# Optimization experiments

Hardware: AMD Instinct MI355X
Metric: run time of the kernel (lower is better)

The kernel has to match this reference:

```python
import jax, jax.numpy as jnp
import numpy as np

TS = 1.5          # hard-coded sampling period in forward()
W_CENTER = 337.927  # hard-coded center frequency in forward()


def shg_mat(yta):
    """Vectorized createSHGmat: yta is a complex64 vector of length N.
    Row m: Ts * fftshift(fft(fftshift(yta * roll(yta, delay[m]) * shiftFactor))).
    torch.roll(x, s)[j] == x[(j - s) % N], matching the gather below."""
    N = yta.shape[0]
    delays_f = jnp.arange(-(N // 2), N // 2, dtype=jnp.float32)
    delays_i = jnp.arange(-(N // 2), N // 2, dtype=jnp.int32)
    shift_factor = jnp.exp(-1j * 2.0 * W_CENTER * TS * delays_f).astype(jnp.complex64)  # [N]
    idx = (jnp.arange(N, dtype=jnp.int32)[None, :] - delays_i[:, None]) % N  # [N, N]
    y_shift = yta[idx]                                    # [N(delay), N(elem)]
    prod = yta[None, :] * y_shift * shift_factor[None, :]  # elementwise, [N, N]
    prod = jnp.fft.fftshift(prod, axes=-1)
    mat = TS * jnp.fft.fftshift(jnp.fft.fft(prod, axis=-1), axes=-1)
    return mat  # complex64 [N, N]


def frog_error(Tref, Tmeas):
    """calcFrogError: scalar FROG error between reference and measured traces."""
    mu = jnp.sum(Tmeas @ Tref) / jnp.sum(Tref @ Tref)
    r = jnp.sum((Tmeas - mu * Tref) ** 2)
    norm = jnp.float32(Tmeas.size) * jnp.max(Tmeas) ** 2
    return jnp.sqrt(r / norm)


def setup_inputs() -> dict:
    key = jax.random.key(0)
    k1, k2, k3 = jax.random.split(key, 3)
    B, N = 8, 1024
    prediction = jax.random.normal(k1, (B, 2 * N), dtype=jnp.float32)
    label = jax.random.normal(k2, (B, 2 * N), dtype=jnp.float32)
    spectrogram = jax.random.uniform(k3, (N, N), dtype=jnp.float32)
    return {"prediction": prediction, "label": label, "spectrogram": spectrogram}


def reference(prediction, label, spectrogram):
    B, two_n = prediction.shape
    n = two_n // 2
    pred_analytical = (prediction[:, :n] + 1j * prediction[:, n:]).astype(jnp.complex64)  # [B, N]
    mats = jax.vmap(shg_mat)(pred_analytical)          # [B, N, N] complex64
    Tref = jnp.abs(mats)                               # predicted SHG trace magnitude
    errs = jax.vmap(lambda t: frog_error(t, spectrogram))(Tref)  # [B]
    # loss = (sum over batch of frog_error) / batch_size; masked MSE terms in the
    # original are computed but never added to the returned loss, so they are omitted.
    return jnp.mean(errs)
```

## Files before the change

kernel.cpp:

```cpp
#include <hip/hip_runtime.h>
#include <math.h>

#define N 1024
#define B_ 8
#define T_ 256
#define R_ 8
#define NREP 4

#define OFF_SF      0
#define OFF_TW      2048
#define OFF_ROWSUM  10240
#define ZERO_START  18432
#define OFF_COLSUMM 18432
#define OFF_SUMM2   19456
#define OFF_MAXM    19457
#define OFF_SUMMT   19464
#define OFF_SUMTT   19472
#define OFF_COLT    20480
#define WS_END      (OFF_COLT + B_ * NREP * N)

#define S1(a) ((a) ^ (((a) >> 2) & 0x10))
#define S2(a) ((a) ^ (((a) >> 3) & 0x0C))
#define S3(a) ((a) ^ (((a) >> 5) & 0x07))
#define S4(a) ((a) ^ (((a) >> 5) & 0x07))

__device__ __forceinline__ float wave_sum(float v) {
    #pragma unroll
    for (int o = 32; o > 0; o >>= 1) v += __shfl_down(v, o, 64);
    return v;
}
__device__ __forceinline__ float wave_max(float v) {
    #pragma unroll
    for (int o = 32; o > 0; o >>= 1) v = fmaxf(v, __shfl_down(v, o, 64));
    return v;
}

__device__ __forceinline__ void load_tw(float tw[6], const float* __restrict__ p) {
    float4 v = *(const float4*)p;
    float2 w = *(const float2*)(p + 4);
    tw[0] = v.x; tw[1] = v.y; tw[2] = v.z; tw[3] = v.w; tw[4] = w.x; tw[5] = w.y;
}

__device__ __forceinline__ void bfly4(float xr[4], float xi[4], const float tw[6]) {
    float t0r = xr[0] + xr[2], t0i = xi[0] + xi[2];
    float t1r = xr[0] - xr[2], t1i = xi[0] - xi[2];
    float t2r = xr[1] + xr[3], t2i = xi[1] + xi[3];
    float t3r = xr[1] - xr[3], t3i = xi[1] - xi[3];
    float y1r = t1r + t3i, y1i = t1i - t3r;
    float y2r = t0r - t2r, y2i = t0i - t2i;
    float y3r = t1r - t3i, y3i = t1i + t3r;
    xr[0] = t0r + t2r;            xi[0] = t0i + t2i;
    xr[1] = y1r * tw[0] - y1i * tw[1]; xi[1] = y1r * tw[1] + y1i * tw[0];
    xr[2] = y2r * tw[2] - y2i * tw[3]; xi[2] = y2r * tw[3] + y2i * tw[2];
    xr[3] = y3r * tw[4] - y3i * tw[5]; xi[3] = y3r * tw[5] + y3i * tw[4];
}

__global__ __launch_bounds__(T_) void k_prep(float* ws) {
    const int e = blockIdx.x * T_ + threadIdx.x;
    {
        double ang = -2.0 * 337.927 * 1.5 * (double)(e - 512);
        double s, c;
        sincos(ang, &s, &c);
        ws[OFF_SF + 2 * e] = (float)c;
        ws[OFF_SF + 2 * e + 1] = (float)s;
    }
    {
        int s = e >> 8, tt = e & 255;
        int h = 256 >> (2 * s);
        int pos = tt & (h - 1);
        int step = 1 << (2 * s);
        double a1 = -2.0 * M_PI * (double)(pos * step) / 1024.0;
        double s1, c1, s2, c2, s3, c3;
        sincos(a1, &s1, &c1);
        sincos(2.0 * a1, &s2, &c2);
        sincos(3.0 * a1, &s3, &c3);
        float* p = ws + OFF_TW + e * 8;
        p[0] = (float)c1; p[1] = (float)s1;
        p[2] = (float)c2; p[3] = (float)s2;
        p[4] = (float)c3; p[5] = (float)s3;
        p[6] = 0.f; p[7] = 0.f;
    }
}

__global__ __launch_bounds__(T_) void k_mstats(const float* __restrict__ M, float* ws) {
    const int t = threadIdx.x;
    const int r0 = blockIdx.x * 16;
    float cs[4] = {0.f, 0.f, 0.f, 0.f};
    float sq = 0.f, mx = 0.f;
    for (int r = 0; r < 16; ++r) {
        const float* row = M + (size_t)(r0 + r) * N;
        #pragma unroll
        for (int q = 0; q < 4; ++q) {
            float v = row[t + T_ * q];
            cs[q] += v;
            sq += v * v;
            mx = fmaxf(mx, v);
        }
    }
    #pragma unroll
    for (int q = 0; q < 4; ++q) atomicAdd(&ws[OFF_COLSUMM + t + T_ * q], cs[q]);
    sq = wave_sum(sq);
    mx = wave_max(mx);
    __shared__ float rs_[4], rm_[4];
    int wid = t >> 6, lane = t & 63;
    if (lane == 0) { rs_[wid] = sq; rm_[wid] = mx; }
    __syncthreads();
    if (t == 0) {
        atomicAdd(&ws[OFF_SUMM2], rs_[0] + rs_[1] + rs_[2] + rs_[3]);
        float X = fmaxf(fmaxf(rm_[0], rm_[1]), fmaxf(rm_[2], rm_[3]));
        atomicMax((unsigned int*)ws + OFF_MAXM, __float_as_uint(X));
    }
}

__global__ __launch_bounds__(T_, 4) void k_row(const float* __restrict__ pred,
                                               const float* __restrict__ M,
                                               float* __restrict__ ws) {
    __shared__ float Yr[N], Yi[N];
    __shared__ float Ar[N], Ai[N], Br[N], Bi[N];
    __shared__ float colA[N];
    __shared__ float red[3][4];
    const int t = threadIdx.x;
    const int m0 = blockIdx.x * R_;
    const int b = blockIdx.y;
    const int wid = t >> 6, lane = t & 63;

    {
        const float* pr = pred + (size_t)b * 2 * N;
        #pragma unroll
        for (int q = 0; q < 4; ++q) {
            int j = t + T_ * q;
            Yr[j] = pr[j];
            Yi[j] = pr[N + j];
            colA[j] = 0.f;
        }
    }
    __syncthreads();

    float mtacc = 0.f, ttacc = 0.f;
    float xr[4], xi[4], tw[6];

    for (int r = 0; r < R_; ++r) {
        const int m = m0 + r;

        {
            const float2* sf2 = (const float2*)(ws + OFF_SF);
            #pragma unroll
            for (int q = 0; q < 4; ++q) {
                int j = t + T_ * q;
                int s = (j - m + 512) & (N - 1);
                float ar = Yr[j], ai = Yi[j];
                float br = Yr[s], bi = Yi[s];
                float2 sv = sf2[j];
                float p_r = ar * br - ai * bi;
                float p_i = ar * bi + ai * br;
                xr[q] = p_r * sv.x - p_i * sv.y;
                xi[q] = p_r * sv.y + p_i * sv.x;
            }
            load_tw(tw, ws + OFF_TW + (size_t)t * 8);
            bfly4(xr, xi, tw);
            #pragma unroll
            for (int q = 0; q < 4; ++q) { int a = t + 256 * q; Ar[a] = xr[q]; Ai[a] = xi[q]; }
        }
        __syncthreads();

        {
            int base = ((t >> 6) << 8) | (t & 63);
            #pragma unroll
            for (int q = 0; q < 4; ++q) { int a = base + (q << 6); xr[q] = Ar[a]; xi[q] = Ai[a]; }
            load_tw(tw, ws + OFF_TW + (size_t)(256 + t) * 8);
            bfly4(xr, xi, tw);
            #pragma unroll
            for (int q = 0; q < 4; ++q) { int a = S1(base + (q << 6)); Br[a] = xr[q]; Bi[a] = xi[q]; }
        }
        __syncthreads();

        {
            int base = ((t >> 4) << 6) | (t & 15);
            #pragma unroll
            for (int q = 0; q < 4; ++q) { int a = S1(base + (q << 4)); xr[q] = Br[a]; xi[q] = Bi[a]; }
            load_tw(tw, ws + OFF_TW + (size_t)(512 + t) * 8);
            bfly4(xr, xi, tw);
            #pragma unroll
            for (int q = 0; q < 4; ++q) { int a = S2(base + (q << 4)); Ar[a] = xr[q]; Ai[a] = xi[q]; }
        }
        __syncthreads();

        {
            int base = ((t >> 2) << 4) | (t & 3);
            #pragma unroll
            for (int q = 0; q < 4; ++q) { int a = S2(base + (q << 2)); xr[q] = Ar[a]; xi[q] = Ai[a]; }
            load_tw(tw, ws + OFF_TW + (size_t)(768 + t) * 8);
            bfly4(xr, xi, tw);
            #pragma unroll
            for (int q = 0; q < 4; ++q) { int a = S3(base + (q << 2)); Br[a] = xr[q]; Bi[a] = xi[q]; }
        }
        __syncthreads();

        {
            int base = t << 2;
            #pragma unroll
            for (int q = 0; q < 4; ++q) { int a = S3(base + q); xr[q] = Br[a]; xi[q] = Bi[a]; }
            float t0r = xr[0] + xr[2], t0i = xi[0] + xi[2];
            float t1r = xr[0] - xr[2], t1i = xi[0] - xi[2];
            float t2r = xr[1] + xr[3], t2i = xi[1] + xi[3];
            float t3r = xr[1] - xr[3], t3i = xi[1] - xi[3];
            float yr[4], yi[4];
            yr[0] = t0r + t2r; yi[0] = t0i + t2i;
            yr[1] = t1r + t3i; yi[1] = t1i - t3r;
            yr[2] = t0r - t2r; yi[2] = t0i - t2i;
            yr[3] = t1r - t3i; yi[3] = t1i + t3r;
            int r4t = ((t & 3) << 6) | (((t >> 2) & 3) << 4) | (((t >> 4) & 3) << 2) | ((t >> 6) & 3);
            #pragma unroll
            for (int q = 0; q < 4; ++q) {
                int c = ((q << 8) | r4t) ^ 512;
                Ar[S4(c)] = 1.5f * sqrtf(yr[q] * yr[q] + yi[q] * yi[q]);
            }
        }
        __syncthreads();

        {
            const float* Mrow = M + (size_t)m * N;
            float rs = 0.f;
            #pragma unroll
            for (int q = 0; q < 4; ++q) {
                int cc = t + 256 * q;
                float v = Ar[S4(cc)];
                rs += v;
                ttacc += v * v;
                mtacc += Mrow[cc] * v;
                colA[cc] += v;
            }
            rs = wave_sum(rs);
            if (lane == 0) red[0][wid] = rs;
            __syncthreads();
            if (t == 0) {
                ws[OFF_ROWSUM + b * N + m] = red[0][0] + red[0][1] + red[0][2] + red[0][3];
            }
        }
    }

    {
        float* colT = ws + OFF_COLT + (size_t)(b * NREP + (blockIdx.x & (NREP - 1))) * N;
        #pragma unroll
        for (int q = 0; q < 4; ++q) {
            int cc = t + 256 * q;
            atomicAdd(&colT[cc], colA[cc]);
        }
        float mt = wave_sum(mtacc);
        float tt2 = wave_sum(ttacc);
        if (lane == 0) { red[1][wid] = mt; red[2][wid] = tt2; }
        __syncthreads();
        if (t == 0) {
            atomicAdd(&ws[OFF_SUMMT + b], red[1][0] + red[1][1] + red[1][2] + red[1][3]);
            atomicAdd(&ws[OFF_SUMTT + b], red[2][0] + red[2][1] + red[2][2] + red[2][3]);
        }
    }
}

__global__ __launch_bounds__(T_) void k_final(float* ws, float* out) {
    __shared__ double redn[4], redd[4];
    const int b = blockIdx.x;
    const int t = threadIdx.x;
    const int wid = t >> 6, lane = t & 63;
    const float* rowsum = ws + OFF_ROWSUM + (size_t)b * N;
    double num = 0.0, den = 0.0;
    #pragma unroll
    for (int q = 0; q < 4; ++q) {
        int j = t + 256 * q;
        double r = (double)rowsum[j];
        float ct = 0.f;
        #pragma unroll
        for (int rep = 0; rep < NREP; ++rep)
            ct += ws[OFF_COLT + (size_t)(b * NREP + rep) * N + j];
        num += (double)ws[OFF_COLSUMM + j] * r;
        den += (double)ct * r;
    }
    #pragma unroll
    for (int o = 32; o > 0; o >>= 1) {
        num += __shfl_down(num, o, 64);
        den += __shfl_down(den, o, 64);
    }
    if (lane == 0) { redn[wid] = num; redd[wid] = den; }
    __syncthreads();
    if (t == 0) {
        double NUM = redn[0] + redn[1] + redn[2] + redn[3];
        double DEN = redd[0] + redd[1] + redd[2] + redd[3];
        double mu = NUM / DEN;
        double r = (double)ws[OFF_SUMM2] - 2.0 * mu * (double)ws[OFF_SUMMT + b]
                 + mu * mu * (double)ws[OFF_SUMTT + b];
        float mx = ws[OFF_MAXM];
        double norm = 1048576.0 * (double)mx * (double)mx;
        atomicAdd(out, (float)(sqrt(r / norm) / 8.0));
    }
}

extern "C" void kernel_launch(void* const* d_in, const int* in_sizes, int n_in,
                              void* d_out, int out_size, void* d_ws, size_t ws_size,
                              hipStream_t stream) {
    const float* pred = (const float*)d_in[0];
    const float* M = (const float*)d_in[2];
    float* ws = (float*)d_ws;
    float* out = (float*)d_out;

    hipMemsetAsync(ws + ZERO_START, 0, (size_t)(WS_END - ZERO_START) * sizeof(float), stream);
    hipMemsetAsync(out, 0, sizeof(float), stream);
    k_prep<<<4, T_, 0, stream>>>(ws);
    k_mstats<<<64, T_, 0, stream>>>(M, ws);
    dim3 grid(N / R_, B_);
    k_row<<<grid, T_, 0, stream>>>(pred, M, ws);
    k_final<<<B_, T_, 0, stream>>>(ws, out);
}
```

Before: 106.0 us.

## Exploit row symmetry m↔N−m, fuse M stats into row kernel, drop memsets

Uses the magnitude symmetry between delay rows m and N−m so each block computes only rows 0..512 and reuses the FFT magnitudes for the mirrored row, weighting the trace sums accordingly. The spectrogram statistics (column sums, sum of squares, max) move from a separate kernel into the batch-0 blocks of the row kernel, and the workspace and output zeroing moves from memset calls into the prep kernel. Together these cut the FFT work roughly in half and remove three launches. In exchange the b==0 blocks read two M rows and carry extra branches, and the grid now has 129 columns with an uneven final block.

Result: no change. 105.3 us (-0.6%).

```diff
diff --git a/kernel.cpp b/kernel.cpp
--- a/kernel.cpp
+++ b/kernel.cpp
@@ -4,8 +4,9 @@
 #define N 1024
 #define B_ 8
 #define T_ 256
-#define R_ 8
+#define R_ 4
 #define NREP 4
+#define GX 129
 
 #define OFF_SF      0
 #define OFF_TW      2048
@@ -55,7 +56,7 @@
     xr[3] = y3r * tw[4] - y3i * tw[5]; xi[3] = y3r * tw[5] + y3i * tw[4];
 }
 
-__global__ __launch_bounds__(T_) void k_prep(float* ws) {
+__global__ __launch_bounds__(T_) void k_prep(float* ws, float* out) {
     const int e = blockIdx.x * T_ + threadIdx.x;
     {
         double ang = -2.0 * 337.927 * 1.5 * (double)(e - 512);
@@ -80,36 +81,8 @@
         p[4] = (float)c3; p[5] = (float)s3;
         p[6] = 0.f; p[7] = 0.f;
     }
-}
-
-__global__ __launch_bounds__(T_) void k_mstats(const float* __restrict__ M, float* ws) {
-    const int t = threadIdx.x;
-    const int r0 = blockIdx.x * 16;
-    float cs[4] = {0.f, 0.f, 0.f, 0.f};
-    float sq = 0.f, mx = 0.f;
-    for (int r = 0; r < 16; ++r) {
-        const float* row = M + (size_t)(r0 + r) * N;
-        #pragma unroll
-        for (int q = 0; q < 4; ++q) {
-            float v = row[t + T_ * q];
-            cs[q] += v;
-            sq += v * v;
-            mx = fmaxf(mx, v);
-        }
-    }
-    #pragma unroll
-    for (int q = 0; q < 4; ++q) atomicAdd(&ws[OFF_COLSUMM + t + T_ * q], cs[q]);
-    sq = wave_sum(sq);
-    mx = wave_max(mx);
-    __shared__ float rs_[4], rm_[4];
-    int wid = t >> 6, lane = t & 63;
-    if (lane == 0) { rs_[wid] = sq; rm_[wid] = mx; }
-    __syncthreads();
-    if (t == 0) {
-        atomicAdd(&ws[OFF_SUMM2], rs_[0] + rs_[1] + rs_[2] + rs_[3]);
-        float X = fmaxf(fmaxf(rm_[0], rm_[1]), fmaxf(rm_[2], rm_[3]));
-        atomicMax((unsigned int*)ws + OFF_MAXM, __float_as_uint(X));
-    }
+    for (int j = ZERO_START + e; j < WS_END; j += 4 * T_) ws[j] = 0.f;
+    if (e == 0) out[0] = 0.f;
 }
 
 __global__ __launch_bounds__(T_, 4) void k_row(const float* __restrict__ pred,
@@ -117,11 +90,13 @@
                                                float* __restrict__ ws) {
     __shared__ float Yr[N], Yi[N];
     __shared__ float Ar[N], Ai[N], Br[N], Bi[N];
-    __shared__ float colA[N];
-    __shared__ float red[3][4];
+    __shared__ float colA[N], colM[N];
+    __shared__ float red[5][4];
     const int t = threadIdx.x;
-    const int m0 = blockIdx.x * R_;
+    const int blk = blockIdx.x;
     const int b = blockIdx.y;
+    const int nr = (blk == GX - 1) ? 1 : R_;
+    const int m0 = blk * R_;
     const int wid = t >> 6, lane = t & 63;
 
     {
@@ -132,15 +107,18 @@
             Yr[j] = pr[j];
             Yi[j] = pr[N + j];
             colA[j] = 0.f;
+            colM[j] = 0.f;
         }
     }
     __syncthreads();
 
-    float mtacc = 0.f, ttacc = 0.f;
+    float mtacc = 0.f, ttacc = 0.f, sqacc = 0.f, mxacc = 0.f;
     float xr[4], xi[4], tw[6];
 
-    for (int r = 0; r < R_; ++r) {
+    for (int r = 0; r < nr; ++r) {
         const int m = m0 + r;
+        const int mm = (N - m) & (N - 1);
+        const float w = (mm == m) ? 1.f : 2.f;
 
         {
             const float2* sf2 = (const float2*)(ws + OFF_SF);
@@ -220,39 +198,72 @@
 
         {
             const float* Mrow = M + (size_t)m * N;
+            const float* Mrow2 = M + (size_t)mm * N;
             float rs = 0.f;
             #pragma unroll
             for (int q = 0; q < 4; ++q) {
                 int cc = t + 256 * q;
                 float v = Ar[S4(cc)];
                 rs += v;
-                ttacc += v * v;
-                mtacc += Mrow[cc] * v;
-                colA[cc] += v;
+                ttacc += w * v * v;
+                float m1 = Mrow[cc];
+                float msum = m1;
+                if (mm != m) msum += Mrow2[cc];
+                mtacc += msum * v;
+                colA[cc] += w * v;
+                if (b == 0) {
+                    colM[cc] += msum;
+                    sqacc += m1 * m1;
+                    mxacc = fmaxf(mxacc, m1);
+                    if (mm != m) {
+                        float m2 = msum - m1;
+                        sqacc += m2 * m2;
+                        mxacc = fmaxf(mxacc, m2);
+                    }
+                }
             }
             rs = wave_sum(rs);
             if (lane == 0) red[0][wid] = rs;
             __syncthreads();
             if (t == 0) {
-                ws[OFF_ROWSUM + b * N + m] = red[0][0] + red[0][1] + red[0][2] + red[0][3];
+                float R = red[0][0] + red[0][1] + red[0][2] + red[0][3];
+                ws[OFF_ROWSUM + b * N + m] = R;
+                if (mm != m) ws[OFF_ROWSUM + b * N + mm] = R;
             }
         }
     }
 
     {
-        float* colT = ws + OFF_COLT + (size_t)(b * NREP + (blockIdx.x & (NREP - 1))) * N;
+        float* colT = ws + OFF_COLT + (size_t)(b * NREP + (blk & (NREP - 1))) * N;
         #pragma unroll
         for (int q = 0; q < 4; ++q) {
             int cc = t + 256 * q;
             atomicAdd(&colT[cc], colA[cc]);
         }
+        if (b == 0) {
+            #pragma unroll
+            for (int q = 0; q < 4; ++q) {
+                int cc = t + 256 * q;
+                atomicAdd(&ws[OFF_COLSUMM + cc], colM[cc]);
+            }
+        }
         float mt = wave_sum(mtacc);
         float tt2 = wave_sum(ttacc);
         if (lane == 0) { red[1][wid] = mt; red[2][wid] = tt2; }
+        if (b == 0) {
+            float sq = wave_sum(sqacc);
+            float mx = wave_max(mxacc);
+            if (lane == 0) { red[3][wid] = sq; red[4][wid] = mx; }
+        }
         __syncthreads();
         if (t == 0) {
             atomicAdd(&ws[OFF_SUMMT + b], red[1][0] + red[1][1] + red[1][2] + red[1][3]);
             atomicAdd(&ws[OFF_SUMTT + b], red[2][0] + red[2][1] + red[2][2] + red[2][3]);
+            if (b == 0) {
+                atomicAdd(&ws[OFF_SUMM2], red[3][0] + red[3][1] + red[3][2] + red[3][3]);
+                float X = fmaxf(fmaxf(red[4][0], red[4][1]), fmaxf(red[4][2], red[4][3]));
+                atomicMax((unsigned int*)ws + OFF_MAXM, __float_as_uint(X));
+            }
         }
     }
 }
@@ -302,11 +313,8 @@
     float* ws = (float*)d_ws;
     float* out = (float*)d_out;
 
-    hipMemsetAsync(ws + ZERO_START, 0, (size_t)(WS_END - ZERO_START) * sizeof(float), stream);
-    hipMemsetAsync(out, 0, sizeof(float), stream);
-    k_prep<<<4, T_, 0, stream>>>(ws);
-    k_mstats<<<64, T_, 0, stream>>>(M, ws);
-    dim3 grid(N / R_, B_);
+    k_prep<<<4, T_, 0, stream>>>(ws, out);
+    dim3 grid(GX, B_);
     k_row<<<grid, T_, 0, stream>>>(pred, M, ws);
     k_final<<<B_, T_, 0, stream>>>(ws, out);
 }
```
